# Performance work log

Hardware: AMD Instinct MI355X
Metric: run time of the kernel (lower is better)

## Reference

```python
import jax, jax.numpy as jnp
import numpy as np

# Vanilla tanh-RNN (num_layers=1, batch_first) followed by tanh + dropout(eval: identity) + linear.

def setup_inputs() -> dict:
    key = jax.random.key(0)
    ks = jax.random.split(key, 7)
    B, T, I, H, C = 16384, 64, 64, 100, 40
    s_ih = 1.0 / np.sqrt(H)
    return {
        "x": jax.random.normal(ks[0], (B, T * I), dtype=jnp.float32),
        "W_ih": jax.random.normal(ks[1], (H, I), dtype=jnp.float32) * s_ih,
        "W_hh": jax.random.normal(ks[2], (H, H), dtype=jnp.float32) * s_ih,
        "b_ih": jax.random.normal(ks[3], (H,), dtype=jnp.float32) * s_ih,
        "b_hh": jax.random.normal(ks[4], (H,), dtype=jnp.float32) * s_ih,
        "fc_W": jax.random.normal(ks[5], (C, H), dtype=jnp.float32) * 0.1,
        "fc_b": jax.random.normal(ks[6], (C,), dtype=jnp.float32) * 0.1,
    }


def reference(x, W_ih, W_hh, b_ih, b_hh, fc_W, fc_b):
    B = x.shape[0]
    x = x.reshape(B, 64, 64)  # [B, T, I]
    # Precompute input projections for all steps in one GEMM: [B, T, H]
    xp = jnp.einsum("bti,hi->bth", x, W_ih) + b_ih + b_hh
    h0 = jnp.zeros((B, W_hh.shape[0]), dtype=x.dtype)

    def step(h, xp_t):  # h: [B, H], xp_t: [B, H]
        h_new = jnp.tanh(xp_t + h @ W_hh.T)
        return h_new, None

    h_last, _ = jax.lax.scan(step, h0, jnp.swapaxes(xp, 0, 1))  # scan over T
    out = jnp.tanh(h_last)  # tanh on last-step output
    # dropout(p=0.2) in eval mode = identity
    return out @ fc_W.T + fc_b  # [B, 40]
```

## Files before the change

kernel.cpp:

```cpp
#include <hip/hip_runtime.h>


typedef _Float16 half8 __attribute__((ext_vector_type(8)));
typedef float float4_t __attribute__((ext_vector_type(4)));

#define SLOT_BYTES 5120
#define GLOAD16(gp, lp)                                                   \
  __builtin_amdgcn_global_load_lds(                                       \
      (const __attribute__((address_space(1))) void*)(gp),                \
      (__attribute__((address_space(3))) void*)(lp), 16, 0, 0)

__device__ __forceinline__ float tanh_fast(float x) {
  float e = __builtin_amdgcn_exp2f(x * 2.8853900817779268f);
  return 1.0f - 2.0f * __builtin_amdgcn_rcpf(e + 1.0f);
}

__global__ __launch_bounds__(256, 1) void rnn_fused(
    const float* __restrict__ x, const float* __restrict__ W_ih,
    const float* __restrict__ W_hh, const float* __restrict__ b_ih,
    const float* __restrict__ b_hh, const float* __restrict__ fc_W,
    const float* __restrict__ fc_b, float* __restrict__ out, int B)
{
  __shared__ char ring[4][4 * SLOT_BYTES];
  const int lane = threadIdx.x & 63;
  const int wave = threadIdx.x >> 6;
  const int g = lane >> 4;
  const int c = lane & 15;
  const int rowbase = (blockIdx.x * 4 + wave) * 16;
  char* ring_w = &ring[wave][0];
  const unsigned int ring_base =
      (unsigned int)(uintptr_t)(__attribute__((address_space(3))) char*)ring_w;

  half8 wih[2][7];
  half8 whh[4][7];
  float4_t bias[7];

  #pragma unroll
  for (int nt = 0; nt < 7; ++nt) {
    int nb = nt * 16 + 4 * g;
    float4_t bi = {0.f, 0.f, 0.f, 0.f};
    if (nb + 3 < 100) {
      float4_t a = *(const float4_t*)(b_ih + nb);
      float4_t b = *(const float4_t*)(b_hh + nb);
      bi = a + b;
    }
    bias[nt] = bi;

    int nrow = nt * 16 + c;
    bool rv = (nrow < 100);
    #pragma unroll
    for (int kb = 0; kb < 2; ++kb) {
      float4_t f0 = {0.f,0.f,0.f,0.f}, f1 = {0.f,0.f,0.f,0.f};
      if (rv) {
        const float* p = W_ih + nrow * 64 + kb * 32 + g * 8;
        f0 = *(const float4_t*)p;
        f1 = *(const float4_t*)(p + 4);
      }
      half8 h;
      #pragma unroll
      for (int j = 0; j < 4; ++j) { h[j] = (_Float16)f0[j]; h[4 + j] = (_Float16)f1[j]; }
      wih[kb][nt] = h;
    }
    #pragma unroll
    for (int kb = 0; kb < 4; ++kb) {
      int clo = kb * 32 + 4 * g;
      int chi = clo + 16;
      float4_t f0 = {0.f,0.f,0.f,0.f}, f1 = {0.f,0.f,0.f,0.f};
      if (rv && clo + 3 < 100) f0 = *(const float4_t*)(W_hh + nrow * 100 + clo);
      if (rv && chi + 3 < 100) f1 = *(const float4_t*)(W_hh + nrow * 100 + chi);
      half8 h;
      #pragma unroll
      for (int j = 0; j < 4; ++j) { h[j] = (_Float16)f0[j]; h[4 + j] = (_Float16)f1[j]; }
      whh[kb][nt] = h;
    }
  }

  const float* gsrc[5];
  #pragma unroll
  for (int j = 0; j < 5; ++j) {
    int m = j * 64 + lane;
    int r = (m * 3856) >> 16;
    int c17 = m - r * 17;
    bool valid = (r < 16) & (c17 < 16);
    int row = rowbase + (valid ? r : 0);
    int col = valid ? c17 * 4 : 0;
    gsrc[j] = x + (size_t)row * 4096 + col;
  }

  #pragma unroll
  for (int s = 0; s < 3; ++s)
    #pragma unroll
    for (int j = 0; j < 5; ++j)
      GLOAD16(gsrc[j] + s * 64, ring_w + s * SLOT_BYTES + j * 1024);

  float4_t acc[7];
  half8 hfrag[4];
  #pragma unroll
  for (int kb = 0; kb < 4; ++kb) hfrag[kb] = (half8)(_Float16)0.0f;

  const unsigned int roff = (unsigned)(c * 272 + g * 32);

  for (int t = 0; t < 64; ++t) {
    int tp = t + 3; if (tp > 63) tp = 63;
    char* lb = ring_w + ((t + 3) & 3) * SLOT_BYTES;
    #pragma unroll
    for (int j = 0; j < 5; ++j)
      GLOAD16(gsrc[j] + tp * 64, lb + j * 1024);

    asm volatile("s_waitcnt vmcnt(15)" ::: "memory");

    unsigned int a = ring_base + (unsigned)((t & 3) * SLOT_BYTES) + roff;
    float4_t s0, s1, s2, s3;
    asm volatile(
        "ds_read_b128 %0, %4 offset:0\n\t"
        "ds_read_b128 %1, %4 offset:16\n\t"
        "ds_read_b128 %2, %4 offset:128\n\t"
        "ds_read_b128 %3, %4 offset:144\n\t"
        "s_waitcnt lgkmcnt(0)"
        : "=&v"(s0), "=&v"(s1), "=&v"(s2), "=&v"(s3)
        : "v"(a));
    __builtin_amdgcn_sched_barrier(0);

    #pragma unroll
    for (int nt = 0; nt < 7; ++nt)
      acc[nt] = __builtin_amdgcn_mfma_f32_16x16x32_f16(whh[0][nt], hfrag[0], bias[nt], 0, 0, 0);
    #pragma unroll
    for (int kb = 1; kb < 4; ++kb)
      #pragma unroll
      for (int nt = 0; nt < 7; ++nt)
        acc[nt] = __builtin_amdgcn_mfma_f32_16x16x32_f16(whh[kb][nt], hfrag[kb], acc[nt], 0, 0, 0);

    half8 xb0, xb1;
    #pragma unroll
    for (int j = 0; j < 4; ++j) {
      xb0[j] = (_Float16)s0[j]; xb0[4 + j] = (_Float16)s1[j];
      xb1[j] = (_Float16)s2[j]; xb1[4 + j] = (_Float16)s3[j];
    }
    #pragma unroll
    for (int nt = 0; nt < 7; ++nt) {
      acc[nt] = __builtin_amdgcn_mfma_f32_16x16x32_f16(wih[0][nt], xb0, acc[nt], 0, 0, 0);
      acc[nt] = __builtin_amdgcn_mfma_f32_16x16x32_f16(wih[1][nt], xb1, acc[nt], 0, 0, 0);
    }

    #pragma unroll
    for (int nt = 0; nt < 7; ++nt)
      #pragma unroll
      for (int v = 0; v < 4; ++v)
        acc[nt][v] = tanh_fast(acc[nt][v]);

    #pragma unroll
    for (int kb = 0; kb < 4; ++kb) {
      half8 h;
      #pragma unroll
      for (int v = 0; v < 4; ++v) {
        h[v] = (_Float16)acc[2 * kb][v];
        h[4 + v] = (kb < 3) ? (_Float16)acc[2 * kb + 1][v] : (_Float16)0.0f;
      }
      hfrag[kb] = h;
    }
  }

  #pragma unroll
  for (int nt = 0; nt < 7; ++nt)
    #pragma unroll
    for (int v = 0; v < 4; ++v)
      acc[nt][v] = tanh_fast(acc[nt][v]);
  #pragma unroll
  for (int kb = 0; kb < 4; ++kb) {
    half8 h;
    #pragma unroll
    for (int v = 0; v < 4; ++v) {
      h[v] = (_Float16)acc[2 * kb][v];
      h[4 + v] = (kb < 3) ? (_Float16)acc[2 * kb + 1][v] : (_Float16)0.0f;
    }
    hfrag[kb] = h;
  }

  half8 wfc[4][3];
  float4_t bfc[3];
  #pragma unroll
  for (int nt = 0; nt < 3; ++nt) {
    int nb = nt * 16 + 4 * g;
    float4_t bi = {0.f,0.f,0.f,0.f};
    if (nb + 3 < 40) bi = *(const float4_t*)(fc_b + nb);
    bfc[nt] = bi;

    int nrow = nt * 16 + c;
    bool rv = (nrow < 40);
    #pragma unroll
    for (int kb = 0; kb < 4; ++kb) {
      int clo = kb * 32 + 4 * g;
      int chi = clo + 16;
      float4_t f0 = {0.f,0.f,0.f,0.f}, f1 = {0.f,0.f,0.f,0.f};
      if (rv && clo + 3 < 100) f0 = *(const float4_t*)(fc_W + nrow * 100 + clo);
      if (rv && chi + 3 < 100) f1 = *(const float4_t*)(fc_W + nrow * 100 + chi);
      half8 h;
      #pragma unroll
      for (int j = 0; j < 4; ++j) { h[j] = (_Float16)f0[j]; h[4 + j] = (_Float16)f1[j]; }
      wfc[kb][nt] = h;
    }
  }

  float4_t oacc[3];
  #pragma unroll
  for (int nt = 0; nt < 3; ++nt) oacc[nt] = bfc[nt];
  #pragma unroll
  for (int kb = 0; kb < 4; ++kb)
    #pragma unroll
    for (int nt = 0; nt < 3; ++nt)
      oacc[nt] = __builtin_amdgcn_mfma_f32_16x16x32_f16(wfc[kb][nt], hfrag[kb], oacc[nt], 0, 0, 0);

  #pragma unroll
  for (int nt = 0; nt < 3; ++nt)
    #pragma unroll
    for (int v = 0; v < 4; ++v) {
      int n = nt * 16 + 4 * g + v;
      if (n < 40)
        out[(size_t)(rowbase + c) * 40 + n] = oacc[nt][v];
    }
}

extern "C" void kernel_launch(void* const* d_in, const int* in_sizes, int n_in,
                              void* d_out, int out_size, void* d_ws, size_t ws_size,
                              hipStream_t stream) {
  const float* x    = (const float*)d_in[0];
  const float* W_ih = (const float*)d_in[1];
  const float* W_hh = (const float*)d_in[2];
  const float* b_ih = (const float*)d_in[3];
  const float* b_hh = (const float*)d_in[4];
  const float* fc_W = (const float*)d_in[5];
  const float* fc_b = (const float*)d_in[6];
  float* outp = (float*)d_out;

  int B = in_sizes[0] / 4096;
  int grid = (B + 63) / 64;
  rnn_fused<<<grid, 256, 0, stream>>>(x, W_ih, W_hh, b_ih, b_hh, fc_W, fc_b, outp, B);
}
```

Measured before the change: 67.59 us.

## Use single-wave blocks with double-buffered 4-timestep x slabs in LDS

Each block becomes one wave handling 16 rows, and x is staged through LDS in 1 KB-per-row slabs covering four timesteps, double-buffered. Each lane issues 16 contiguous global-to-LDS loads per slab instead of five scattered loads per timestep. This coarsens the prefetch granularity and lets more small blocks share a CU. The cost is a more bursty load schedule, a wait at the start of each group of four steps, and a refill that waits on the buffer just consumed.

```diff
diff --git a/kernel.cpp b/kernel.cpp
--- a/kernel.cpp
+++ b/kernel.cpp
@@ -4,7 +4,8 @@
 typedef _Float16 half8 __attribute__((ext_vector_type(8)));
 typedef float float4_t __attribute__((ext_vector_type(4)));
 
-#define SLOT_BYTES 5120
+#define ROW_BYTES 1088
+#define BUF_BYTES (16 * ROW_BYTES)
 #define GLOAD16(gp, lp)                                                   \
   __builtin_amdgcn_global_load_lds(                                       \
       (const __attribute__((address_space(1))) void*)(gp),                \
@@ -15,21 +16,26 @@
   return 1.0f - 2.0f * __builtin_amdgcn_rcpf(e + 1.0f);
 }
 
-__global__ __launch_bounds__(256, 1) void rnn_fused(
+__device__ __forceinline__ void issue_slab(const float* srcl, int slab, char* buf) {
+  const float* s = srcl + slab * 256;
+  #pragma unroll
+  for (int j = 0; j < 16; ++j) {
+    GLOAD16(s, buf + j * ROW_BYTES);
+    s += 4096;
+  }
+}
+
+__global__ __launch_bounds__(64, 1) void rnn_fused(
     const float* __restrict__ x, const float* __restrict__ W_ih,
     const float* __restrict__ W_hh, const float* __restrict__ b_ih,
     const float* __restrict__ b_hh, const float* __restrict__ fc_W,
     const float* __restrict__ fc_b, float* __restrict__ out, int B)
 {
-  __shared__ char ring[4][4 * SLOT_BYTES];
+  __shared__ char xring[2 * BUF_BYTES];
   const int lane = threadIdx.x & 63;
-  const int wave = threadIdx.x >> 6;
   const int g = lane >> 4;
   const int c = lane & 15;
-  const int rowbase = (blockIdx.x * 4 + wave) * 16;
-  char* ring_w = &ring[wave][0];
-  const unsigned int ring_base =
-      (unsigned int)(uintptr_t)(__attribute__((address_space(3))) char*)ring_w;
+  const int rowbase = blockIdx.x * 16;
 
   half8 wih[2][7];
   half8 whh[4][7];
@@ -75,89 +81,79 @@
     }
   }
 
-  const float* gsrc[5];
-  #pragma unroll
-  for (int j = 0; j < 5; ++j) {
-    int m = j * 64 + lane;
-    int r = (m * 3856) >> 16;
-    int c17 = m - r * 17;
-    bool valid = (r < 16) & (c17 < 16);
-    int row = rowbase + (valid ? r : 0);
-    int col = valid ? c17 * 4 : 0;
-    gsrc[j] = x + (size_t)row * 4096 + col;
-  }
-
-  #pragma unroll
-  for (int s = 0; s < 3; ++s)
-    #pragma unroll
-    for (int j = 0; j < 5; ++j)
-      GLOAD16(gsrc[j] + s * 64, ring_w + s * SLOT_BYTES + j * 1024);
+  const float* srcl = x + (size_t)rowbase * 4096 + lane * 4;
+
+  issue_slab(srcl, 0, xring);
+  issue_slab(srcl, 1, xring + BUF_BYTES);
+
+  const unsigned ring_base =
+      (unsigned)(uintptr_t)(__attribute__((address_space(3))) char*)xring;
+  const unsigned xa0 = ring_base + (unsigned)(c * ROW_BYTES + g * 32);
 
   float4_t acc[7];
   half8 hfrag[4];
   #pragma unroll
   for (int kb = 0; kb < 4; ++kb) hfrag[kb] = (half8)(_Float16)0.0f;
 
-  const unsigned int roff = (unsigned)(c * 272 + g * 32);
-
-  for (int t = 0; t < 64; ++t) {
-    int tp = t + 3; if (tp > 63) tp = 63;
-    char* lb = ring_w + ((t + 3) & 3) * SLOT_BYTES;
-    #pragma unroll
-    for (int j = 0; j < 5; ++j)
-      GLOAD16(gsrc[j] + tp * 64, lb + j * 1024);
-
-    asm volatile("s_waitcnt vmcnt(15)" ::: "memory");
-
-    unsigned int a = ring_base + (unsigned)((t & 3) * SLOT_BYTES) + roff;
-    float4_t s0, s1, s2, s3;
-    asm volatile(
-        "ds_read_b128 %0, %4 offset:0\n\t"
-        "ds_read_b128 %1, %4 offset:16\n\t"
-        "ds_read_b128 %2, %4 offset:128\n\t"
-        "ds_read_b128 %3, %4 offset:144\n\t"
-        "s_waitcnt lgkmcnt(0)"
-        : "=&v"(s0), "=&v"(s1), "=&v"(s2), "=&v"(s3)
-        : "v"(a));
-    __builtin_amdgcn_sched_barrier(0);
-
-    #pragma unroll
-    for (int nt = 0; nt < 7; ++nt)
-      acc[nt] = __builtin_amdgcn_mfma_f32_16x16x32_f16(whh[0][nt], hfrag[0], bias[nt], 0, 0, 0);
-    #pragma unroll
-    for (int kb = 1; kb < 4; ++kb)
+  for (int grp = 0; grp < 16; ++grp) {
+    asm volatile("s_waitcnt vmcnt(16)" ::: "memory");
+    unsigned xg = xa0 + (unsigned)((grp & 1) * BUF_BYTES);
+
+    #pragma unroll
+    for (int t4 = 0; t4 < 4; ++t4) {
+      unsigned xs = xg + (unsigned)(t4 * 256);
+      float4_t s0, s1, s2, s3;
+      asm volatile(
+          "ds_read_b128 %0, %4 offset:0\n\t"
+          "ds_read_b128 %1, %4 offset:16\n\t"
+          "ds_read_b128 %2, %4 offset:128\n\t"
+          "ds_read_b128 %3, %4 offset:144\n\t"
+          "s_waitcnt lgkmcnt(0)"
+          : "=&v"(s0), "=&v"(s1), "=&v"(s2), "=&v"(s3)
+          : "v"(xs) : "memory");
+      __builtin_amdgcn_sched_barrier(0);
+
       #pragma unroll
       for (int nt = 0; nt < 7; ++nt)
-        acc[nt] = __builtin_amdgcn_mfma_f32_16x16x32_f16(whh[kb][nt], hfrag[kb], acc[nt], 0, 0, 0);
-
-    half8 xb0, xb1;
-    #pragma unroll
-    for (int j = 0; j < 4; ++j) {
-      xb0[j] = (_Float16)s0[j]; xb0[4 + j] = (_Float16)s1[j];
-      xb1[j] = (_Float16)s2[j]; xb1[4 + j] = (_Float16)s3[j];
-    }
-    #pragma unroll
-    for (int nt = 0; nt < 7; ++nt) {
-      acc[nt] = __builtin_amdgcn_mfma_f32_16x16x32_f16(wih[0][nt], xb0, acc[nt], 0, 0, 0);
-      acc[nt] = __builtin_amdgcn_mfma_f32_16x16x32_f16(wih[1][nt], xb1, acc[nt], 0, 0, 0);
-    }
-
-    #pragma unroll
-    for (int nt = 0; nt < 7; ++nt)
-      #pragma unroll
-      for (int v = 0; v < 4; ++v)
-        acc[nt][v] = tanh_fast(acc[nt][v]);
-
-    #pragma unroll
-    for (int kb = 0; kb < 4; ++kb) {
-      half8 h;
-      #pragma unroll
-      for (int v = 0; v < 4; ++v) {
-        h[v] = (_Float16)acc[2 * kb][v];
-        h[4 + v] = (kb < 3) ? (_Float16)acc[2 * kb + 1][v] : (_Float16)0.0f;
-      }
-      hfrag[kb] = h;
-    }
+        acc[nt] = __builtin_amdgcn_mfma_f32_16x16x32_f16(whh[0][nt], hfrag[0], bias[nt], 0, 0, 0);
+      #pragma unroll
+      for (int kb = 1; kb < 4; ++kb)
+        #pragma unroll
+        for (int nt = 0; nt < 7; ++nt)
+          acc[nt] = __builtin_amdgcn_mfma_f32_16x16x32_f16(whh[kb][nt], hfrag[kb], acc[nt], 0, 0, 0);
+
+      half8 xb0, xb1;
+      #pragma unroll
+      for (int j = 0; j < 4; ++j) {
+        xb0[j] = (_Float16)s0[j]; xb0[4 + j] = (_Float16)s1[j];
+        xb1[j] = (_Float16)s2[j]; xb1[4 + j] = (_Float16)s3[j];
+      }
+      #pragma unroll
+      for (int nt = 0; nt < 7; ++nt) {
+        acc[nt] = __builtin_amdgcn_mfma_f32_16x16x32_f16(wih[0][nt], xb0, acc[nt], 0, 0, 0);
+        acc[nt] = __builtin_amdgcn_mfma_f32_16x16x32_f16(wih[1][nt], xb1, acc[nt], 0, 0, 0);
+      }
+
+      #pragma unroll
+      for (int nt = 0; nt < 7; ++nt)
+        #pragma unroll
+        for (int v = 0; v < 4; ++v)
+          acc[nt][v] = tanh_fast(acc[nt][v]);
+
+      #pragma unroll
+      for (int kb = 0; kb < 4; ++kb) {
+        half8 h;
+        #pragma unroll
+        for (int v = 0; v < 4; ++v) {
+          h[v] = (_Float16)acc[2 * kb][v];
+          h[4 + v] = (kb < 3) ? (_Float16)acc[2 * kb + 1][v] : (_Float16)0.0f;
+        }
+        hfrag[kb] = h;
+      }
+    }
+
+    int sl = grp + 2; if (sl > 15) sl = 15;
+    issue_slab(srcl, sl, xring + (grp & 1) * BUF_BYTES);
   }
 
   #pragma unroll
@@ -233,6 +229,6 @@
   float* outp = (float*)d_out;
 
   int B = in_sizes[0] / 4096;
-  int grid = (B + 63) / 64;
-  rnn_fused<<<grid, 256, 0, stream>>>(x, W_ih, W_hh, b_ih, b_hh, fc_W, fc_b, outp, B);
-}
+  int grid = (B + 15) / 16;
+  rnn_fused<<<grid, 64, 0, stream>>>(x, W_ih, W_hh, b_ih, b_hh, fc_W, fc_b, outp, B);
+}
```

New measurement: 65.31 us, median of 2. -3.4%, faster.
